# Performance work log

Hardware: AMD Instinct MI355X
Metric: run time of the kernel (lower is better)

The kernel has to match this reference:

```python
import jax, jax.numpy as jnp
import numpy as np

B, S, E = 4, 2048, 1024

def setup_inputs() -> dict:
    key = jax.random.key(0)
    ks = jax.random.split(key, 7)
    sc = 1.0 / np.sqrt(E)
    return {
        "x": jax.random.normal(ks[0], (B, S, E), dtype=jnp.float32),
        "wq_w": jax.random.normal(ks[1], (E, E), dtype=jnp.float32) * sc,
        "wq_b": jax.random.normal(ks[2], (E,), dtype=jnp.float32) * 0.01,
        "wk_w": jax.random.normal(ks[3], (E, E), dtype=jnp.float32) * sc,
        "wk_b": jax.random.normal(ks[4], (E,), dtype=jnp.float32) * 0.01,
        "wv_w": jax.random.normal(ks[5], (E, E), dtype=jnp.float32) * sc,
        "wv_b": jax.random.normal(ks[6], (E,), dtype=jnp.float32) * 0.01,
    }

def reference(x, wq_w, wq_b, wk_w, wk_b, wv_w, wv_b):
    # Linear projections (torch nn.Linear: y = x @ W^T + b)
    Q = jnp.einsum('bse,fe->bsf', x, wq_w) + wq_b
    K = jnp.einsum('bse,fe->bsf', x, wk_w) + wk_b
    V = jnp.einsum('bse,fe->bsf', x, wv_w) + wv_b
    # scaled dot-product attention, full [B, S, S] scores (single head)
    scores = jnp.einsum('bqe,bke->bqk', Q, K) / jnp.sqrt(jnp.asarray(Q.shape[-1], Q.dtype))
    attn = jax.nn.softmax(scores, axis=-1)
    return jnp.einsum('bqk,bke->bqe', attn, V)
```

## Files before the change

kernel.cpp:

```cpp
#include <hip/hip_runtime.h>
#include <hip/hip_bf16.h>
#include <stdint.h>

#define B_ 4
#define S_ 2048
#define E_ 1024

typedef __bf16 bf16;
typedef __attribute__((ext_vector_type(8))) __bf16 bf16x8;
typedef __attribute__((ext_vector_type(4))) float f32x4;
typedef __attribute__((ext_vector_type(4))) float float4v;
typedef __attribute__((ext_vector_type(4))) unsigned int uint4v;
typedef __attribute__((ext_vector_type(4))) unsigned short ushort4v;

__device__ inline unsigned short f2bf(float f) {
  union { float f; unsigned int u; } c; c.f = f;
  unsigned int u = c.u;
  unsigned int r = (u + 0x7FFFu + ((u >> 16) & 1u)) >> 16;
  return (unsigned short)r;
}

__device__ inline void load16_to_lds(const void* g, void* l) {
  __builtin_amdgcn_global_load_lds(
      (const __attribute__((address_space(1))) void*)g,
      (__attribute__((address_space(3))) void*)l,
      16, 0, 0);
}

__global__ __launch_bounds__(256) void cvt_all(
    const float* __restrict__ x, const float* __restrict__ w0,
    const float* __restrict__ w1, const float* __restrict__ w2,
    unsigned short* __restrict__ out) {
  const long off = (long)blockIdx.x * 256 + threadIdx.x;
  const float* in;
  long ibase;
  if (blockIdx.x < 8192)       { in = x;  ibase = 0; }
  else if (blockIdx.x < 9216)  { in = w0; ibase = 8192L * 256; }
  else if (blockIdx.x < 10240) { in = w1; ibase = 9216L * 256; }
  else                         { in = w2; ibase = 10240L * 256; }
  float4v f = ((const float4v*)in)[off - ibase];
  ushort4v o;
  o.x = f2bf(f.x); o.y = f2bf(f.y); o.z = f2bf(f.z); o.w = f2bf(f.w);
  ((ushort4v*)out)[off] = o;
}


#define MFMA_(a, b, c) __builtin_amdgcn_mfma_f32_16x16x32_bf16(a, b, c, 0, 0, 0)

#define STAGE_A8(kh, buf, kofs)                                         \
  { char* d_ = smem + (buf) * 65536 + (kh) * 16384 + wj;                \
    load16_to_lds(pA0 + (kofs) + (kh) * 32, d_);                        \
    load16_to_lds(pA1 + (kofs) + (kh) * 32, d_ + 1024); }

#define STAGE_B8(kh, buf, kofs)                                         \
  { char* d_ = smem + (buf) * 65536 + 32768 + (kh) * 16384 + wj;        \
    load16_to_lds(pB0 + (kofs) + (kh) * 32, d_);                        \
    load16_to_lds(pB1 + (kofs) + (kh) * 32, d_ + 1024); }

#define PH_READS(mh, kh)                                                \
    const char* rb_ = smem + cur * 65536 + (kh) * 16384;                \
    bf16x8 a0_ = *(const bf16x8*)(rb_ + offA[(mh) * 4 + 0]);            \
    bf16x8 a1_ = *(const bf16x8*)(rb_ + offA[(mh) * 4 + 1]);            \
    bf16x8 a2_ = *(const bf16x8*)(rb_ + offA[(mh) * 4 + 2]);            \
    bf16x8 a3_ = *(const bf16x8*)(rb_ + offA[(mh) * 4 + 3]);            \
    bf16x8 b0_ = *(const bf16x8*)(rb_ + offB[0]);                       \
    bf16x8 b1_ = *(const bf16x8*)(rb_ + offB[1]);                       \
    bf16x8 b2_ = *(const bf16x8*)(rb_ + offB[2]);                       \
    bf16x8 b3_ = *(const bf16x8*)(rb_ + offB[3])

#define PH_TAIL(mh)                                                     \
    __builtin_amdgcn_s_barrier();                                       \
    asm volatile("s_waitcnt lgkmcnt(0)" ::: "memory");                  \
    __builtin_amdgcn_s_setprio(1);                                      \
    acc[(mh)*4+0][0] = MFMA_(a0_, b0_, acc[(mh)*4+0][0]);               \
    acc[(mh)*4+0][1] = MFMA_(a0_, b1_, acc[(mh)*4+0][1]);               \
    acc[(mh)*4+0][2] = MFMA_(a0_, b2_, acc[(mh)*4+0][2]);               \
    acc[(mh)*4+0][3] = MFMA_(a0_, b3_, acc[(mh)*4+0][3]);               \
    acc[(mh)*4+1][0] = MFMA_(a1_, b0_, acc[(mh)*4+1][0]);               \
    acc[(mh)*4+1][1] = MFMA_(a1_, b1_, acc[(mh)*4+1][1]);               \
    acc[(mh)*4+1][2] = MFMA_(a1_, b2_, acc[(mh)*4+1][2]);               \
    acc[(mh)*4+1][3] = MFMA_(a1_, b3_, acc[(mh)*4+1][3]);               \
    acc[(mh)*4+2][0] = MFMA_(a2_, b0_, acc[(mh)*4+2][0]);               \
    acc[(mh)*4+2][1] = MFMA_(a2_, b1_, acc[(mh)*4+2][1]);               \
    acc[(mh)*4+2][2] = MFMA_(a2_, b2_, acc[(mh)*4+2][2]);               \
    acc[(mh)*4+2][3] = MFMA_(a2_, b3_, acc[(mh)*4+2][3]);               \
    acc[(mh)*4+3][0] = MFMA_(a3_, b0_, acc[(mh)*4+3][0]);               \
    acc[(mh)*4+3][1] = MFMA_(a3_, b1_, acc[(mh)*4+3][1]);               \
    acc[(mh)*4+3][2] = MFMA_(a3_, b2_, acc[(mh)*4+3][2]);               \
    acc[(mh)*4+3][3] = MFMA_(a3_, b3_, acc[(mh)*4+3][3]);               \
    __builtin_amdgcn_s_setprio(0);                                      \
    __builtin_amdgcn_s_barrier();

template <int MODE>
__global__ __launch_bounds__(512, 2) void gemm8(
    const bf16* __restrict__ A, const bf16* __restrict__ B, void* __restrict__ Cv,
    const float* __restrict__ bias, const float* __restrict__ bias_b,
    const float* __restrict__ bias_v, unsigned short* __restrict__ VtOut,
    float* __restrict__ rowsum,
    int M, int N, int K, int lda, int ldb, int ldc,
    long sA, long sB, long sC, float scale) {
  (void)M; (void)N;
  __shared__ __align__(128) char smem[131072];
  const int tid = threadIdx.x;
  const int wave = tid >> 6;
  const int lane = tid & 63;
  const int lrow = lane & 15;
  const int quad = lane >> 4;
  const int xt = blockIdx.x, yt = blockIdx.y, zb = blockIdx.z;
  A += (long)zb * sA;
  B += (long)zb * sB;
  const int row0 = yt * 256;
  const int col0 = xt * 256;
  const int wm = (wave >> 2) * 128;
  const int wn = (wave & 3) * 64;
  const int wj = wave * 2048;

  const bf16* pA0; const bf16* pA1; const bf16* pB0; const bf16* pB1;
  {
    int r0 = wave * 2048 + lane * 16;
    int l0 = r0 ^ (((r0 >> 7) & 7) << 4);
    int x0 = l0 >> 6;
    int g0 = (l0 >> 4) & 3;
    int r1 = r0 + 1024;
    int l1 = r1 ^ (((r1 >> 7) & 7) << 4);
    int x1 = l1 >> 6;
    int g1 = (l1 >> 4) & 3;
    pA0 = A + (long)(row0 + x0) * lda + g0 * 8;
    pA1 = A + (long)(row0 + x1) * lda + g1 * 8;
    pB0 = B + (long)(col0 + x0) * ldb + g0 * 8;
    pB1 = B + (long)(col0 + x1) * ldb + g1 * 8;
  }

  int offA[8], offB[4];
#pragma unroll
  for (int mh = 0; mh < 2; ++mh)
#pragma unroll
    for (int f = 0; f < 4; ++f) {
      int x = wm + mh * 64 + f * 16 + lrow;
      int rb = ((x >> 1) << 7) + ((x & 1) << 6) + (quad << 4);
      offA[mh * 4 + f] = rb ^ (((x >> 1) & 7) << 4);
    }
#pragma unroll
  for (int n = 0; n < 4; ++n) {
    int y = wn + n * 16 + lrow;
    int rb = ((y >> 1) << 7) + ((y & 1) << 6) + (quad << 4);
    offB[n] = (rb ^ (((y >> 1) & 7) << 4)) + 32768;
  }

  f32x4 acc[8][4] = {};
  const int nt = K >> 6;

  STAGE_A8(0, 0, 0); STAGE_B8(0, 0, 0);
  STAGE_A8(1, 0, 0); STAGE_B8(1, 0, 0);
  STAGE_A8(0, 1, 64); STAGE_B8(0, 1, 64);
  asm volatile("s_waitcnt vmcnt(8)" ::: "memory");
  __builtin_amdgcn_s_barrier();

  for (int u = 0; u < nt; ++u) {
    const int cur = u & 1;
    const int nxt = cur ^ 1;
    const int ks = u << 6;
    const bool st1 = (u + 1 < nt);
    const bool st2 = (u + 2 < nt);
    {
      PH_READS(0, 0);
      if (st1) STAGE_A8(1, nxt, ks + 64);
      PH_TAIL(0);
    }
    {
      PH_READS(1, 0);
      if (st1) STAGE_B8(1, nxt, ks + 64);
      if (st1) { asm volatile("s_waitcnt vmcnt(8)" ::: "memory"); }
      else     { asm volatile("s_waitcnt vmcnt(0)" ::: "memory"); }
      PH_TAIL(1);
    }
    {
      PH_READS(0, 1);
      if (st2) STAGE_A8(0, cur, ks + 128);
      PH_TAIL(0);
    }
    {
      PH_READS(1, 1);
      if (st2) STAGE_B8(0, cur, ks + 128);
      if (st2)                 { asm volatile("s_waitcnt vmcnt(8)" ::: "memory"); }
      else if (u == nt - 2)    { asm volatile("s_waitcnt vmcnt(4)" ::: "memory"); }
      PH_TAIL(1);
    }
  }

  if constexpr (MODE == 8) {
    float* C = (float*)Cv + (long)zb * sC;
    const float* rs = rowsum + (long)zb * S_;
#pragma unroll
    for (int m = 0; m < 8; ++m) {
#pragma unroll
      for (int r = 0; r < 4; ++r) {
        const int row = row0 + wm + m * 16 + quad * 4 + r;
        const float inv = 1.0f / rs[row];
#pragma unroll
        for (int n = 0; n < 4; ++n) {
          const int col = col0 + wn + n * 16 + lrow;
          C[(long)row * ldc + col] = acc[m][n][r] * inv;
        }
      }
    }
  } else if constexpr (MODE == 7) {
    unsigned short* C = (unsigned short*)Cv + (long)zb * sC;
    float* rs = rowsum + (long)zb * S_;
    float rsump[8][4];
#pragma unroll
    for (int m = 0; m < 8; ++m)
#pragma unroll
      for (int r = 0; r < 4; ++r) rsump[m][r] = 0.f;
#pragma unroll
    for (int n = 0; n < 4; ++n) {
      const int col = col0 + wn + n * 16 + lrow;
#pragma unroll
      for (int m = 0; m < 8; ++m) {
#pragma unroll
        for (int r = 0; r < 4; ++r) {
          const int row = row0 + wm + m * 16 + quad * 4 + r;
          const float e = __expf(acc[m][n][r] * scale);
          rsump[m][r] += e;
          C[(long)row * ldc + col] = f2bf(e);
        }
      }
    }
#pragma unroll
    for (int m = 0; m < 8; ++m) {
#pragma unroll
      for (int r = 0; r < 4; ++r) {
        float v = rsump[m][r];
        v += __shfl_xor(v, 1);
        v += __shfl_xor(v, 2);
        v += __shfl_xor(v, 4);
        v += __shfl_xor(v, 8);
        if (lrow == 0)
          atomicAdd(&rs[row0 + wm + m * 16 + quad * 4 + r], v);
      }
    }
  } else {
    if (col0 < 2048) {
      unsigned short* C = (unsigned short*)Cv;
#pragma unroll
      for (int n = 0; n < 4; ++n) {
        const int col = col0 + wn + n * 16 + lrow;
        const float bcol = (col < E_) ? bias[col] : bias_b[col - E_];
#pragma unroll
        for (int m = 0; m < 8; ++m) {
#pragma unroll
          for (int r = 0; r < 4; ++r) {
            const int row = row0 + wm + m * 16 + quad * 4 + r;
            C[(long)row * ldc + col] = f2bf(acc[m][n][r] + bcol);
          }
        }
      }
    } else {
#pragma unroll
      for (int n = 0; n < 4; ++n) {
        const int e = col0 + wn + n * 16 + lrow - 2048;
        const float bv_ = bias_v[e];
#pragma unroll
        for (int m = 0; m < 8; ++m) {
          const int row = row0 + wm + m * 16 + quad * 4;
          ushort4v o;
          o.x = f2bf(acc[m][n][0] + bv_);
          o.y = f2bf(acc[m][n][1] + bv_);
          o.z = f2bf(acc[m][n][2] + bv_);
          o.w = f2bf(acc[m][n][3] + bv_);
          *(ushort4v*)(VtOut + (long)e * (B_ * S_) + row) = o;
        }
      }
    }
  }
}

template <int MODE, int SWZ, int NXT>
__global__ __launch_bounds__(256, 4) void gemm_bt(
    const bf16* __restrict__ A, const bf16* __restrict__ B, void* __restrict__ Cv,
    const float* __restrict__ bias, const float* __restrict__ bias_b,
    const float* __restrict__ bias_v, unsigned short* __restrict__ VtOut,
    float* __restrict__ rowsum,
    int M, int N, int K, int lda, int ldb, int ldc,
    long sA, long sB, long sC, float scale, int nyt) {
  __shared__ bf16 As[128 * 64];
  __shared__ bf16 Bs[128 * 64];

  int xt, yt, zb;
  if (SWZ == 0) {
    xt = blockIdx.x; yt = blockIdx.y; zb = blockIdx.z;
  } else {
    const int flat = blockIdx.x;
    const int xcd = flat & 7;
    const int local = flat >> 3;
    zb = xcd >> 1;
    const int w = (xcd & 1) * (NXT * nyt / 2) + local;
    xt = w % NXT; yt = w / NXT;
  }

  A += (long)zb * sA;
  B += (long)zb * sB;
  const int tid = threadIdx.x;
  const int wave = tid >> 6;
  const int lane = tid & 63;
  const int lrow = lane & 15;
  const int quad = lane >> 4;
  const int row0 = yt * 128;
  const int col0 = xt * 128;
  const int wm = (wave >> 1) * 64;
  const int wn = (wave & 1) * 64;

  f32x4 acc[4][4] = {};

  const int r0 = wave * 8 + (lane >> 3);
  const int c0 = (lane & 7) * 8;

  const bf16* pA0 = A + (long)(row0 + r0) * lda + c0;
  const bf16* pA1 = pA0 + 32L * lda;
  const bf16* pA2 = pA0 + 64L * lda;
  const bf16* pA3 = pA0 + 96L * lda;
  const bf16* pB0 = B + (long)(col0 + r0) * ldb + c0;
  const bf16* pB1 = pB0 + 32L * ldb;
  const bf16* pB2 = pB0 + 64L * ldb;
  const bf16* pB3 = pB0 + 96L * ldb;
  bf16* ldsA = As + wave * 512;
  bf16* ldsB = Bs + wave * 512;

  for (int ks = 0; ks < K; ks += 64) {
    load16_to_lds(pA0, ldsA);
    load16_to_lds(pA1, ldsA + 2048);
    load16_to_lds(pA2, ldsA + 4096);
    load16_to_lds(pA3, ldsA + 6144);
    load16_to_lds(pB0, ldsB);
    load16_to_lds(pB1, ldsB + 2048);
    load16_to_lds(pB2, ldsB + 4096);
    load16_to_lds(pB3, ldsB + 6144);
    __syncthreads();
#pragma unroll
    for (int kk = 0; kk < 64; kk += 32) {
      bf16x8 af[4], bfr[4];
#pragma unroll
      for (int i = 0; i < 4; ++i)
        af[i] = *(const bf16x8*)(As + (wm + i * 16 + lrow) * 64 + kk + quad * 8);
#pragma unroll
      for (int j = 0; j < 4; ++j)
        bfr[j] = *(const bf16x8*)(Bs + (wn + j * 16 + lrow) * 64 + kk + quad * 8);
#pragma unroll
      for (int i = 0; i < 4; ++i)
#pragma unroll
        for (int j = 0; j < 4; ++j)
          acc[i][j] = __builtin_amdgcn_mfma_f32_16x16x32_bf16(af[i], bfr[j], acc[i][j], 0, 0, 0);
    }
    __syncthreads();
    pA0 += 64; pA1 += 64; pA2 += 64; pA3 += 64;
    pB0 += 64; pB1 += 64; pB2 += 64; pB3 += 64;
  }

  if (MODE == 8) {
    float* C = (float*)Cv + (long)zb * sC;
    const float* rs = rowsum + (long)zb * S_;
#pragma unroll
    for (int i = 0; i < 4; ++i) {
#pragma unroll
      for (int r = 0; r < 4; ++r) {
        const int row = row0 + wm + i * 16 + quad * 4 + r;
        const float inv = 1.0f / rs[row];
#pragma unroll
        for (int j = 0; j < 4; ++j) {
          const int col = col0 + wn + j * 16 + lrow;
          C[(long)row * ldc + col] = acc[i][j][r] * inv;
        }
      }
    }
  } else if (MODE == 7) {
    unsigned short* C = (unsigned short*)Cv + (long)zb * sC;
    float* rs = rowsum + (long)zb * S_;
    float rsump[4][4];
#pragma unroll
    for (int i = 0; i < 4; ++i)
#pragma unroll
      for (int r = 0; r < 4; ++r) rsump[i][r] = 0.f;
#pragma unroll
    for (int j = 0; j < 4; ++j) {
      const int col = col0 + wn + j * 16 + lrow;
#pragma unroll
      for (int i = 0; i < 4; ++i) {
#pragma unroll
        for (int r = 0; r < 4; ++r) {
          const int row = row0 + wm + i * 16 + quad * 4 + r;
          const float e = __expf(acc[i][j][r] * scale);
          rsump[i][r] += e;
          C[(long)row * ldc + col] = f2bf(e);
        }
      }
    }
#pragma unroll
    for (int i = 0; i < 4; ++i) {
#pragma unroll
      for (int r = 0; r < 4; ++r) {
        float v = rsump[i][r];
        v += __shfl_xor(v, 1);
        v += __shfl_xor(v, 2);
        v += __shfl_xor(v, 4);
        v += __shfl_xor(v, 8);
        if (lrow == 0)
          atomicAdd(&rs[row0 + wm + i * 16 + quad * 4 + r], v);
      }
    }
  } else {
    if (col0 < 2048) {
      unsigned short* C = (unsigned short*)Cv;
#pragma unroll
      for (int j = 0; j < 4; ++j) {
        const int col = col0 + wn + j * 16 + lrow;
        const float bcol = (col < E_) ? bias[col] : bias_b[col - E_];
#pragma unroll
        for (int i = 0; i < 4; ++i) {
#pragma unroll
          for (int r = 0; r < 4; ++r) {
            const int row = row0 + wm + i * 16 + quad * 4 + r;
            C[(long)row * ldc + col] = f2bf(acc[i][j][r] + bcol);
          }
        }
      }
    } else {
#pragma unroll
      for (int j = 0; j < 4; ++j) {
        const int e = col0 + wn + j * 16 + lrow - 2048;
        const float bv_ = bias_v[e];
#pragma unroll
        for (int i = 0; i < 4; ++i) {
          const int row = row0 + wm + i * 16 + quad * 4;
          ushort4v o;
          o.x = f2bf(acc[i][j][0] + bv_);
          o.y = f2bf(acc[i][j][1] + bv_);
          o.z = f2bf(acc[i][j][2] + bv_);
          o.w = f2bf(acc[i][j][3] + bv_);
          *(ushort4v*)(VtOut + (long)e * (B_ * S_) + row) = o;
        }
      }
    }
  }
}

extern "C" void kernel_launch(void* const* d_in, const int* in_sizes, int n_in,
                              void* d_out, int out_size, void* d_ws, size_t ws_size,
                              hipStream_t stream) {
  const float* x    = (const float*)d_in[0];
  const float* wq_w = (const float*)d_in[1];
  const float* wq_b = (const float*)d_in[2];
  const float* wk_w = (const float*)d_in[3];
  const float* wk_b = (const float*)d_in[4];
  const float* wv_w = (const float*)d_in[5];
  const float* wv_b = (const float*)d_in[6];
  float* out = (float*)d_out;

  const long NX = (long)B_ * S_ * E_;
  const long NW = (long)E_ * E_;
  char* ws = (char*)d_ws;
  bf16* xb  = (bf16*)ws; ws += NX * 2;
  bf16* wqb = (bf16*)ws; ws += NW * 2;
  bf16* wkb = (bf16*)ws; ws += NW * 2;
  bf16* wvb = (bf16*)ws; ws += NW * 2;
  bf16* QK  = (bf16*)ws; ws += 2 * NX * 2;
  bf16* Vt  = (bf16*)ws; ws += NX * 2;
  bf16* Sc  = (bf16*)ws; ws += (long)B_ * S_ * S_ * 2;
  float* rowsum = (float*)ws; ws += (long)B_ * S_ * 4;

  cvt_all<<<dim3(11264), 256, 0, stream>>>(
      x, wq_w, wk_w, wv_w, (unsigned short*)xb);
  hipMemsetAsync(rowsum, 0, (size_t)B_ * S_ * 4, stream);

  gemm8<6><<<dim3(12, 32, 1), dim3(512), 0, stream>>>(
      xb, wqb, QK, wq_b, wk_b, wv_b, (unsigned short*)Vt, nullptr,
      B_ * S_, 3 * E_, E_, E_, E_, 2 * E_, 0, 0, 0, 1.f);
  gemm8<7><<<dim3(8, 8, 4), dim3(512), 0, stream>>>(
      QK, QK + E_, Sc, nullptr, nullptr, nullptr, nullptr, rowsum,
      S_, S_, E_, 2 * E_, 2 * E_, S_,
      (long)S_ * 2 * E_, (long)S_ * 2 * E_, (long)S_ * S_, 0.03125f);
  dim3 blk(256);
  gemm_bt<8, 1, 8><<<dim3(512, 1, 1), blk, 0, stream>>>(
      Sc, Vt, out, nullptr, nullptr, nullptr, nullptr, rowsum,
      S_, E_, S_, S_, B_ * S_, E_,
      (long)S_ * S_, (long)S_, (long)S_ * E_, 1.f, 16);
}
```

Before: 274.9 us.

## Restructure GEMM main loop into 8-wave ping-pong schedule with new LDS layout

Rewrites the bf16 GEMM mainloop used by all projection and attention matmuls. Each 64-wide K tile is now staged as contiguous 128-row halves with an XOR swizzle. The loop is unrolled by two tiles and split into four MFMA quadrants that reuse A/B fragments across quadrants, with global-to-LDS loads interleaved between them and finer lgkmcnt/vmcnt waits. The aim is to cut redundant LDS reads and hide memory latency behind MFMA work, at the cost of more barriers and a fixed tail that assumes an even tile count of at least four.

```diff
diff --git a/kernel.cpp b/kernel.cpp
--- a/kernel.cpp
+++ b/kernel.cpp
@@ -47,49 +47,55 @@
 
 #define MFMA_(a, b, c) __builtin_amdgcn_mfma_f32_16x16x32_bf16(a, b, c, 0, 0, 0)
 
-#define STAGE_A8(kh, buf, kofs)                                         \
-  { char* d_ = smem + (buf) * 65536 + (kh) * 16384 + wj;                \
-    load16_to_lds(pA0 + (kofs) + (kh) * 32, d_);                        \
-    load16_to_lds(pA1 + (kofs) + (kh) * 32, d_ + 1024); }
-
-#define STAGE_B8(kh, buf, kofs)                                         \
-  { char* d_ = smem + (buf) * 65536 + 32768 + (kh) * 16384 + wj;        \
-    load16_to_lds(pB0 + (kofs) + (kh) * 32, d_);                        \
-    load16_to_lds(pB1 + (kofs) + (kh) * 32, d_ + 1024); }
-
-#define PH_READS(mh, kh)                                                \
-    const char* rb_ = smem + cur * 65536 + (kh) * 16384;                \
-    bf16x8 a0_ = *(const bf16x8*)(rb_ + offA[(mh) * 4 + 0]);            \
-    bf16x8 a1_ = *(const bf16x8*)(rb_ + offA[(mh) * 4 + 1]);            \
-    bf16x8 a2_ = *(const bf16x8*)(rb_ + offA[(mh) * 4 + 2]);            \
-    bf16x8 a3_ = *(const bf16x8*)(rb_ + offA[(mh) * 4 + 3]);            \
-    bf16x8 b0_ = *(const bf16x8*)(rb_ + offB[0]);                       \
-    bf16x8 b1_ = *(const bf16x8*)(rb_ + offB[1]);                       \
-    bf16x8 b2_ = *(const bf16x8*)(rb_ + offB[2]);                       \
-    bf16x8 b3_ = *(const bf16x8*)(rb_ + offB[3])
-
-#define PH_TAIL(mh)                                                     \
-    __builtin_amdgcn_s_barrier();                                       \
-    asm volatile("s_waitcnt lgkmcnt(0)" ::: "memory");                  \
-    __builtin_amdgcn_s_setprio(1);                                      \
-    acc[(mh)*4+0][0] = MFMA_(a0_, b0_, acc[(mh)*4+0][0]);               \
-    acc[(mh)*4+0][1] = MFMA_(a0_, b1_, acc[(mh)*4+0][1]);               \
-    acc[(mh)*4+0][2] = MFMA_(a0_, b2_, acc[(mh)*4+0][2]);               \
-    acc[(mh)*4+0][3] = MFMA_(a0_, b3_, acc[(mh)*4+0][3]);               \
-    acc[(mh)*4+1][0] = MFMA_(a1_, b0_, acc[(mh)*4+1][0]);               \
-    acc[(mh)*4+1][1] = MFMA_(a1_, b1_, acc[(mh)*4+1][1]);               \
-    acc[(mh)*4+1][2] = MFMA_(a1_, b2_, acc[(mh)*4+1][2]);               \
-    acc[(mh)*4+1][3] = MFMA_(a1_, b3_, acc[(mh)*4+1][3]);               \
-    acc[(mh)*4+2][0] = MFMA_(a2_, b0_, acc[(mh)*4+2][0]);               \
-    acc[(mh)*4+2][1] = MFMA_(a2_, b1_, acc[(mh)*4+2][1]);               \
-    acc[(mh)*4+2][2] = MFMA_(a2_, b2_, acc[(mh)*4+2][2]);               \
-    acc[(mh)*4+2][3] = MFMA_(a2_, b3_, acc[(mh)*4+2][3]);               \
-    acc[(mh)*4+3][0] = MFMA_(a3_, b0_, acc[(mh)*4+3][0]);               \
-    acc[(mh)*4+3][1] = MFMA_(a3_, b1_, acc[(mh)*4+3][1]);               \
-    acc[(mh)*4+3][2] = MFMA_(a3_, b2_, acc[(mh)*4+3][2]);               \
-    acc[(mh)*4+3][3] = MFMA_(a3_, b3_, acc[(mh)*4+3][3]);               \
-    __builtin_amdgcn_s_setprio(0);                                      \
-    __builtin_amdgcn_s_barrier();
+#define BAR   asm volatile("s_barrier" ::: "memory")
+#define LGKM0 asm volatile("s_waitcnt lgkmcnt(0)" ::: "memory")
+#define LGKM8 asm volatile("s_waitcnt lgkmcnt(8)" ::: "memory")
+#define VM(n) asm volatile("s_waitcnt vmcnt(" #n ")" ::: "memory")
+
+#define STG_A(H, BUF, tile)                                              \
+  { const bf16* s_ = pAs + (long)(H) * 128 * lda + (long)(tile) * 64;    \
+    char* d_ = sw + (BUF) * 65536 + (H) * 16384;                         \
+    load16_to_lds(s_, d_);                                               \
+    load16_to_lds(s_ + a64, d_ + 8192); }
+
+#define STG_B(H, BUF, tile)                                              \
+  { const bf16* s_ = pBs + (long)(H) * 128 * ldb + (long)(tile) * 64;    \
+    char* d_ = sw + 32768 + (BUF) * 65536 + (H) * 16384;                 \
+    load16_to_lds(s_, d_);                                               \
+    load16_to_lds(s_ + b64, d_ + 8192); }
+
+#define READ_A4(g, BUF)                                                  \
+  { const char* p_ = smem + (BUF) * 65536;                               \
+    af[0][0] = *(const bf16x8*)(p_ + offA[(g) + 0]);                     \
+    af[0][1] = *(const bf16x8*)(p_ + (offA[(g) + 0] ^ 64));              \
+    af[1][0] = *(const bf16x8*)(p_ + offA[(g) + 1]);                     \
+    af[1][1] = *(const bf16x8*)(p_ + (offA[(g) + 1] ^ 64));              \
+    af[2][0] = *(const bf16x8*)(p_ + offA[(g) + 2]);                     \
+    af[2][1] = *(const bf16x8*)(p_ + (offA[(g) + 2] ^ 64));              \
+    af[3][0] = *(const bf16x8*)(p_ + offA[(g) + 3]);                     \
+    af[3][1] = *(const bf16x8*)(p_ + (offA[(g) + 3] ^ 64)); }
+
+#define READ_B2(BF, g, BUF)                                              \
+  { const char* p_ = smem + (BUF) * 65536;                               \
+    BF[0][0] = *(const bf16x8*)(p_ + offB[(g) + 0]);                     \
+    BF[0][1] = *(const bf16x8*)(p_ + (offB[(g) + 0] ^ 64));              \
+    BF[1][0] = *(const bf16x8*)(p_ + offB[(g) + 1]);                     \
+    BF[1][1] = *(const bf16x8*)(p_ + (offB[(g) + 1] ^ 64)); }
+
+#define MM1(m, n, ks, BF) \
+  acc[m][n] = MFMA_(af[(m) & 3][ks], BF[(n) & 1][ks], acc[m][n])
+
+#define MFMA_Q(qm, qn, BF)                                               \
+  __builtin_amdgcn_s_setprio(1);                                         \
+  MM1((qm)*4 + 0, (qn)*2 + 0, 0, BF); MM1((qm)*4 + 0, (qn)*2 + 1, 0, BF);\
+  MM1((qm)*4 + 1, (qn)*2 + 0, 0, BF); MM1((qm)*4 + 1, (qn)*2 + 1, 0, BF);\
+  MM1((qm)*4 + 2, (qn)*2 + 0, 0, BF); MM1((qm)*4 + 2, (qn)*2 + 1, 0, BF);\
+  MM1((qm)*4 + 3, (qn)*2 + 0, 0, BF); MM1((qm)*4 + 3, (qn)*2 + 1, 0, BF);\
+  MM1((qm)*4 + 0, (qn)*2 + 0, 1, BF); MM1((qm)*4 + 0, (qn)*2 + 1, 1, BF);\
+  MM1((qm)*4 + 1, (qn)*2 + 0, 1, BF); MM1((qm)*4 + 1, (qn)*2 + 1, 1, BF);\
+  MM1((qm)*4 + 2, (qn)*2 + 0, 1, BF); MM1((qm)*4 + 2, (qn)*2 + 1, 1, BF);\
+  MM1((qm)*4 + 3, (qn)*2 + 0, 1, BF); MM1((qm)*4 + 3, (qn)*2 + 1, 1, BF);\
+  __builtin_amdgcn_s_setprio(0);
 
 template <int MODE>
 __global__ __launch_bounds__(512, 2) void gemm8(
@@ -113,80 +119,114 @@
   const int col0 = xt * 256;
   const int wm = (wave >> 2) * 128;
   const int wn = (wave & 3) * 64;
-  const int wj = wave * 2048;
-
-  const bf16* pA0; const bf16* pA1; const bf16* pB0; const bf16* pB1;
-  {
-    int r0 = wave * 2048 + lane * 16;
-    int l0 = r0 ^ (((r0 >> 7) & 7) << 4);
-    int x0 = l0 >> 6;
-    int g0 = (l0 >> 4) & 3;
-    int r1 = r0 + 1024;
-    int l1 = r1 ^ (((r1 >> 7) & 7) << 4);
-    int x1 = l1 >> 6;
-    int g1 = (l1 >> 4) & 3;
-    pA0 = A + (long)(row0 + x0) * lda + g0 * 8;
-    pA1 = A + (long)(row0 + x1) * lda + g1 * 8;
-    pB0 = B + (long)(col0 + x0) * ldb + g0 * 8;
-    pB1 = B + (long)(col0 + x1) * ldb + g1 * 8;
+
+  const int srow = tid >> 3;
+  const int sgsrc = ((tid & 7) ^ ((tid >> 3) & 7)) * 8;
+  const bf16* pAs = A + (long)(row0 + srow) * lda + sgsrc;
+  const bf16* pBs = B + (long)(col0 + srow) * ldb + sgsrc;
+  const long a64 = 64L * lda, b64 = 64L * ldb;
+  char* const sw = smem + wave * 1024;
+
+  const int sg = (quad ^ (lrow & 7)) << 4;
+  int offA[8], offB[4];
+#pragma unroll
+  for (int m = 0; m < 8; ++m)
+    offA[m] = (wave >> 2) * 16384 + (m * 16 + lrow) * 128 + sg;
+#pragma unroll
+  for (int n = 0; n < 4; ++n)
+    offB[n] = 32768 + ((wave >> 1) & 1) * 16384 +
+              ((wave & 1) * 64 + n * 16 + lrow) * 128 + sg;
+
+  f32x4 acc[8][4] = {};
+  bf16x8 af[4][2], bfA[2][2], bfB[2][2];
+  const int nt = K >> 6;
+
+  STG_A(0, 0, 0); STG_A(1, 0, 0);
+  STG_B(0, 0, 0); STG_B(1, 0, 0);
+  STG_A(0, 1, 1); STG_A(1, 1, 1);
+  VM(4);
+  BAR;
+
+  for (int u = 0; u + 3 < nt; u += 2) {
+    READ_A4(0, 0); READ_B2(bfA, 0, 0);
+    STG_B(0, 1, u + 1);
+    LGKM8; BAR; LGKM0;
+    MFMA_Q(0, 0, bfA);
+    BAR;
+    READ_B2(bfB, 2, 0);
+    STG_B(1, 1, u + 1);
+    BAR; LGKM0;
+    MFMA_Q(0, 1, bfB);
+    BAR;
+    READ_A4(4, 0);
+    BAR; LGKM0;
+    MFMA_Q(1, 1, bfB);
+    BAR;
+    STG_A(0, 0, u + 2);
+    VM(2);
+    BAR;
+    MFMA_Q(1, 0, bfA);
+    BAR;
+
+    READ_A4(0, 1); READ_B2(bfA, 0, 1);
+    STG_A(1, 0, u + 2); STG_B(0, 0, u + 2);
+    LGKM8; BAR; LGKM0;
+    MFMA_Q(0, 0, bfA);
+    BAR;
+    READ_B2(bfB, 2, 1);
+    STG_B(1, 0, u + 2);
+    BAR; LGKM0;
+    MFMA_Q(0, 1, bfB);
+    BAR;
+    READ_A4(4, 1);
+    BAR; LGKM0;
+    MFMA_Q(1, 1, bfB);
+    BAR;
+    STG_A(0, 1, u + 3); STG_A(1, 1, u + 3);
+    VM(4);
+    BAR;
+    MFMA_Q(1, 0, bfA);
+    BAR;
   }
 
-  int offA[8], offB[4];
-#pragma unroll
-  for (int mh = 0; mh < 2; ++mh)
-#pragma unroll
-    for (int f = 0; f < 4; ++f) {
-      int x = wm + mh * 64 + f * 16 + lrow;
-      int rb = ((x >> 1) << 7) + ((x & 1) << 6) + (quad << 4);
-      offA[mh * 4 + f] = rb ^ (((x >> 1) & 7) << 4);
-    }
-#pragma unroll
-  for (int n = 0; n < 4; ++n) {
-    int y = wn + n * 16 + lrow;
-    int rb = ((y >> 1) << 7) + ((y & 1) << 6) + (quad << 4);
-    offB[n] = (rb ^ (((y >> 1) & 7) << 4)) + 32768;
-  }
-
-  f32x4 acc[8][4] = {};
-  const int nt = K >> 6;
-
-  STAGE_A8(0, 0, 0); STAGE_B8(0, 0, 0);
-  STAGE_A8(1, 0, 0); STAGE_B8(1, 0, 0);
-  STAGE_A8(0, 1, 64); STAGE_B8(0, 1, 64);
-  asm volatile("s_waitcnt vmcnt(8)" ::: "memory");
-  __builtin_amdgcn_s_barrier();
-
-  for (int u = 0; u < nt; ++u) {
-    const int cur = u & 1;
-    const int nxt = cur ^ 1;
-    const int ks = u << 6;
-    const bool st1 = (u + 1 < nt);
-    const bool st2 = (u + 2 < nt);
-    {
-      PH_READS(0, 0);
-      if (st1) STAGE_A8(1, nxt, ks + 64);
-      PH_TAIL(0);
-    }
-    {
-      PH_READS(1, 0);
-      if (st1) STAGE_B8(1, nxt, ks + 64);
-      if (st1) { asm volatile("s_waitcnt vmcnt(8)" ::: "memory"); }
-      else     { asm volatile("s_waitcnt vmcnt(0)" ::: "memory"); }
-      PH_TAIL(1);
-    }
-    {
-      PH_READS(0, 1);
-      if (st2) STAGE_A8(0, cur, ks + 128);
-      PH_TAIL(0);
-    }
-    {
-      PH_READS(1, 1);
-      if (st2) STAGE_B8(0, cur, ks + 128);
-      if (st2)                 { asm volatile("s_waitcnt vmcnt(8)" ::: "memory"); }
-      else if (u == nt - 2)    { asm volatile("s_waitcnt vmcnt(4)" ::: "memory"); }
-      PH_TAIL(1);
-    }
-  }
+  READ_A4(0, 0); READ_B2(bfA, 0, 0);
+  STG_B(0, 1, nt - 1);
+  LGKM8; BAR; LGKM0;
+  MFMA_Q(0, 0, bfA);
+  BAR;
+
+  READ_B2(bfB, 2, 0);
+  STG_B(1, 1, nt - 1);
+  BAR; LGKM0;
+  MFMA_Q(0, 1, bfB);
+  BAR;
+
+  READ_A4(4, 0);
+  BAR; LGKM0;
+  MFMA_Q(1, 1, bfB);
+  BAR;
+
+  VM(0);
+  BAR;
+  MFMA_Q(1, 0, bfA);
+  BAR;
+
+  READ_A4(0, 1); READ_B2(bfA, 0, 1);
+  LGKM8; BAR; LGKM0;
+  MFMA_Q(0, 0, bfA);
+  BAR;
+
+  READ_B2(bfB, 2, 1);
+  BAR; LGKM0;
+  MFMA_Q(0, 1, bfB);
+  BAR;
+
+  READ_A4(4, 1);
+  BAR; LGKM0;
+  MFMA_Q(1, 1, bfB);
+  BAR;
+
+  MFMA_Q(1, 0, bfA);
 
   if constexpr (MODE == 8) {
     float* C = (float*)Cv + (long)zb * sC;
```

Result: no change. 270.5 us (-1.6%).
